# Kernel tuning notes

Hardware: AMD Instinct MI355X
Metric: run time of the kernel (lower is better)

The kernel has to match this reference:

```python
import jax, jax.numpy as jnp
import numpy as np

N_HEADS = 16
SEG = 64
EPS = 1e-6


def _sigma(x):
    # ELU(x) + 1 kernel feature map (strictly positive)
    return jax.nn.elu(x) + 1.0


def setup_inputs() -> dict:
    key = jax.random.key(0)
    kx, kq, kk, kv, ko = jax.random.split(key, 5)
    B, T, D = 4, 4096, 1024
    scale = D ** -0.5
    return {
        "x": jax.random.normal(kx, (B, T, D), dtype=jnp.float32),
        "W_q": jax.random.normal(kq, (D, D), dtype=jnp.float32) * scale,
        "W_k": jax.random.normal(kk, (D, D), dtype=jnp.float32) * scale,
        "W_v": jax.random.normal(kv, (D, D), dtype=jnp.float32) * scale,
        "W_o": jax.random.normal(ko, (D, D), dtype=jnp.float32) * scale,
        "beta_param": jnp.zeros((N_HEADS,), dtype=jnp.float32),
    }


def _infini_attention(x, W_q, W_k, W_v, W_o, beta_param):
    B, T, D = x.shape
    H = N_HEADS
    dk = D // H
    assert T % SEG == 0
    S = T // SEG

    def proj(W):
        # nn.Linear: x @ W.T ; split heads -> (B,H,T,dk) -> (S,B,H,SEG,dk)
        y = (x @ W.T).reshape(B, T, H, dk).transpose(0, 2, 1, 3)
        return y.reshape(B, H, S, SEG, dk).transpose(2, 0, 1, 3, 4)

    Qs, Ks, Vs = proj(W_q), proj(W_k), proj(W_v)

    beta = jax.nn.sigmoid(beta_param).reshape(1, H, 1, 1)
    causal = jnp.triu(jnp.ones((SEG, SEG), dtype=bool), k=1)
    inv_sqrt_dk = 1.0 / jnp.sqrt(jnp.asarray(dk, x.dtype))

    M0 = jnp.zeros((B, H, dk, dk), dtype=x.dtype)
    z0 = jnp.zeros((B, H, dk), dtype=x.dtype)

    def step(carry, qkv):
        M, z = carry
        q, k, v = qkv  # each (B,H,SEG,dk)
        # Eq.4 memory retrieval
        sq = _sigma(q)
        denom_q = jnp.sum(sq * z[:, :, None, :], axis=-1, keepdims=True) + EPS
        A_mem = jnp.matmul(sq, M) / denom_q
        # local causal softmax attention
        scores = jnp.matmul(q, jnp.swapaxes(k, -2, -1)) * inv_sqrt_dk
        scores = jnp.where(causal, -jnp.inf, scores)
        A_dot = jnp.matmul(jax.nn.softmax(scores, axis=-1), v)
        A_s = beta * A_mem + (1.0 - beta) * A_dot
        # Eq.5 delta-rule memory update
        sk = _sigma(k)
        denom_k = jnp.sum(sk * z[:, :, None, :], axis=-1, keepdims=True) + EPS
        V_prev = jnp.matmul(sk, M) / denom_k
        M_new = M + jnp.einsum("bhtk,bhtv->bhkv", sk, v - V_prev)
        z_new = z + jnp.sum(sk, axis=-2)
        return (M_new, z_new), A_s

    (M, z), outs = jax.lax.scan(step, (M0, z0), (Qs, Ks, Vs))
    # outs: (S,B,H,SEG,dk) -> (B,T,D)
    out = outs.transpose(1, 3, 0, 2, 4).reshape(B, S * SEG, H, dk)
    # careful: need segment-major time ordering -> (B, H, T, dk) then (B,T,H,dk)
    out = outs.transpose(1, 2, 0, 3, 4).reshape(B, H, T, dk)
    out = out.transpose(0, 2, 1, 3).reshape(B, T, D)
    out = out @ W_o.T
    return out, M.mean(0), z.mean(0)


def reference(x, W_q, W_k, W_v, W_o, beta_param):
    return _infini_attention(x, W_q, W_k, W_v, W_o, beta_param)
```

## Files before the change

### kernel.cpp

```cpp
#include <hip/hip_runtime.h>

typedef __bf16 bf16_t;
typedef __bf16 bf16x8 __attribute__((ext_vector_type(8)));
typedef __bf16 bf16x4 __attribute__((ext_vector_type(4)));
typedef float  f32x4  __attribute__((ext_vector_type(4)));

#define QKV_STR 3072

__device__ __forceinline__ void gload16(const bf16_t* g, bf16_t* l) {
    __builtin_amdgcn_global_load_lds(
        (const __attribute__((address_space(1))) void*)(g),
        (__attribute__((address_space(3))) void*)(l), 16, 0, 0);
}

__global__ __launch_bounds__(256) void cast_bf16_kernel(const float* __restrict__ in,
                                                        bf16_t* __restrict__ out, int n4) {
    int i = blockIdx.x * 256 + threadIdx.x;
    if (i >= n4) return;
    f32x4 v = *reinterpret_cast<const f32x4*>(in + (size_t)i * 4);
    bf16x4 o;
    o[0] = (bf16_t)v[0]; o[1] = (bf16_t)v[1]; o[2] = (bf16_t)v[2]; o[3] = (bf16_t)v[3];
    *reinterpret_cast<bf16x4*>(out + (size_t)i * 4) = o;
}

__global__ __launch_bounds__(256) void cast4_kernel(const float* __restrict__ w0,
                                                    const float* __restrict__ w1,
                                                    const float* __restrict__ w2,
                                                    const float* __restrict__ w3,
                                                    bf16_t* __restrict__ o0,
                                                    bf16_t* __restrict__ o1,
                                                    bf16_t* __restrict__ o2,
                                                    bf16_t* __restrict__ o3) {
    int which = blockIdx.x >> 10;
    int i = (blockIdx.x & 1023) * 256 + threadIdx.x;
    const float* in = (which == 0) ? w0 : (which == 1) ? w1 : (which == 2) ? w2 : w3;
    bf16_t*     out = (which == 0) ? o0 : (which == 1) ? o1 : (which == 2) ? o2 : o3;
    f32x4 v = *reinterpret_cast<const f32x4*>(in + (size_t)i * 4);
    bf16x4 o;
    o[0] = (bf16_t)v[0]; o[1] = (bf16_t)v[1]; o[2] = (bf16_t)v[2]; o[3] = (bf16_t)v[3];
    *reinterpret_cast<bf16x4*>(out + (size_t)i * 4) = o;
}

__device__ __forceinline__ bf16x8 sigma8(bf16x8 x) {
    bf16x8 o;
#pragma unroll
    for (int j = 0; j < 8; j++) {
        float f = (float)x[j];
        float sg = f > 0.f ? f + 1.f : __expf(f);
        o[j] = (bf16_t)sg;
    }
    return o;
}

template <int OUT_BF16>
__global__ __launch_bounds__(512, 2) void gemm256(const bf16_t* __restrict__ A,
                                                  const bf16_t* __restrict__ Bm,
                                                  void* __restrict__ Cv,
                                                  int M, int N, int K) {
    __shared__ bf16_t As[4][256 * 32];
    __shared__ bf16_t Bs[4][256 * 32];

    int nbn = N >> 8;
    int nwg = (M >> 8) * nbn;
    int bid = blockIdx.x;
    int wg = ((nwg & 7) == 0) ? ((bid & 7) * (nwg >> 3) + (bid >> 3)) : bid;
    int bm = wg / nbn, bn = wg % nbn;

    int tid = threadIdx.x;
    int w = tid >> 6, lane = tid & 63;
    int wm = w >> 2, wn = w & 3;
    int lr = lane & 15, lk = lane >> 4;

    int srow = lane >> 2;
    int schunk = (lane & 3) ^ ((lane >> 3) & 3);
    const bf16_t* gA0 = A  + (size_t)(bm * 256 + w * 32 + srow) * K + schunk * 8;
    const bf16_t* gA1 = gA0 + (size_t)16 * K;
    const bf16_t* gB0 = Bm + (size_t)(bn * 256 + w * 32 + srow) * K + schunk * 8;
    const bf16_t* gB1 = gB0 + (size_t)16 * K;
    int lO0 = (w * 32) * 32 + lane * 8;
    int lO1 = (w * 32 + 16) * 32 + lane * 8;

    int chunkb = (lk ^ ((lr >> 1) & 3)) << 4;
    int aoff[8], boff[4];
#pragma unroll
    for (int mi = 0; mi < 8; mi++) aoff[mi] = (wm * 128 + mi * 16 + lr) * 64 + chunkb;
#pragma unroll
    for (int ni = 0; ni < 4; ni++) boff[ni] = (wn * 64 + ni * 16 + lr) * 64 + chunkb;

    f32x4 acc[8][4];
#pragma unroll
    for (int mi = 0; mi < 8; mi++)
#pragma unroll
        for (int ni = 0; ni < 4; ni++) acc[mi][ni] = (f32x4){0.f, 0.f, 0.f, 0.f};

    const int NT = K >> 5;

    auto STAGE = [&](int t) {
        int slot = t & 3;
        size_t ko = (size_t)t * 32;
        gload16(gA0 + ko, &As[slot][lO0]);
        gload16(gA1 + ko, &As[slot][lO1]);
        gload16(gB0 + ko, &Bs[slot][lO0]);
        gload16(gB1 + ko, &Bs[slot][lO1]);
    };

    STAGE(0); STAGE(1); STAGE(2);

#pragma unroll 1
    for (int t = 0; t < NT; ++t) {
        int ahead = NT - 1 - t;
        if (ahead >= 2)      asm volatile("s_waitcnt vmcnt(8)" ::: "memory");
        else if (ahead == 1) asm volatile("s_waitcnt vmcnt(4)" ::: "memory");
        else                 asm volatile("s_waitcnt vmcnt(0)" ::: "memory");
        __builtin_amdgcn_sched_barrier(0);
        __builtin_amdgcn_s_barrier();
        __builtin_amdgcn_sched_barrier(0);

        const char* pa = (const char*)(&As[t & 3][0]);
        const char* pb = (const char*)(&Bs[t & 3][0]);
        bf16x8 af[8], bfr[4];
#pragma unroll
        for (int mi = 0; mi < 8; mi++)
            af[mi] = *reinterpret_cast<const bf16x8*>(pa + aoff[mi]);
#pragma unroll
        for (int ni = 0; ni < 4; ni++)
            bfr[ni] = *reinterpret_cast<const bf16x8*>(pb + boff[ni]);

        if (t + 3 < NT) STAGE(t + 3);

        asm volatile("s_waitcnt lgkmcnt(0)" ::: "memory");
        __builtin_amdgcn_sched_barrier(0);
        __builtin_amdgcn_s_setprio(1);
#pragma unroll
        for (int mi = 0; mi < 8; mi++)
#pragma unroll
            for (int ni = 0; ni < 4; ni++)
                acc[mi][ni] = __builtin_amdgcn_mfma_f32_16x16x32_bf16(af[mi], bfr[ni], acc[mi][ni], 0, 0, 0);
        __builtin_amdgcn_s_setprio(0);
    }

    int row0 = bm * 256 + wm * 128 + lk * 4;
    int col0 = bn * 256 + wn * 64 + lr;
#pragma unroll
    for (int mi = 0; mi < 8; mi++)
#pragma unroll
        for (int ni = 0; ni < 4; ni++)
#pragma unroll
            for (int jj = 0; jj < 4; jj++) {
                size_t idx = (size_t)(row0 + mi * 16 + jj) * N + (col0 + ni * 16);
                float v = acc[mi][ni][jj];
                if (OUT_BF16) reinterpret_cast<bf16_t*>(Cv)[idx] = (bf16_t)v;
                else          reinterpret_cast<float*>(Cv)[idx]  = v;
            }
}

__global__ __launch_bounds__(256) void attn_kernel(bf16_t* __restrict__ QKV,
                                                   bf16_t* __restrict__ skTg,
                                                   float* __restrict__ csum,
                                                   bf16_t* __restrict__ Adot) {
    __shared__ bf16_t kS[64 * 72];
    __shared__ bf16_t vS[64 * 72];
    __shared__ bf16_t skT[64 * 72];
    __shared__ bf16_t vT[64 * 72];
    __shared__ bf16_t pS[64 * 72];
    __shared__ float  scr[64 * 68];

    int u = blockIdx.x;
    int bh = u >> 6, s = u & 63;
    int b = bh >> 4, h = bh & 15;
    int tid = threadIdx.x;
    int w = tid >> 6, lane = tid & 63;
    int lr = lane & 15, lk = lane >> 4;
    int r = tid >> 2, qd = tid & 3, c0 = qd << 4;

    bf16_t* qp = QKV + (size_t)(b * 4096 + s * 64) * QKV_STR + (size_t)h * 64;
    bf16_t* kp = qp + 1024;
    bf16_t* vp = qp + 2048;
    size_t sb = ((size_t)bh * 64 + s) * 4096;

    {
        bf16x8 k0 = *reinterpret_cast<const bf16x8*>(kp + (size_t)r * QKV_STR + c0);
        bf16x8 k1 = *reinterpret_cast<const bf16x8*>(kp + (size_t)r * QKV_STR + c0 + 8);
        bf16x8 v0 = *reinterpret_cast<const bf16x8*>(vp + (size_t)r * QKV_STR + c0);
        bf16x8 v1 = *reinterpret_cast<const bf16x8*>(vp + (size_t)r * QKV_STR + c0 + 8);
        *reinterpret_cast<bf16x8*>(&kS[r * 72 + c0])     = k0;
        *reinterpret_cast<bf16x8*>(&kS[r * 72 + c0 + 8]) = k1;
        *reinterpret_cast<bf16x8*>(&vS[r * 72 + c0])     = v0;
        *reinterpret_cast<bf16x8*>(&vS[r * 72 + c0 + 8]) = v1;
        bf16x8 s0 = sigma8(k0), s1 = sigma8(k1);
        *reinterpret_cast<bf16x8*>(kp + (size_t)r * QKV_STR + c0)     = s0;
        *reinterpret_cast<bf16x8*>(kp + (size_t)r * QKV_STR + c0 + 8) = s1;
#pragma unroll
        for (int j = 0; j < 8; j++) {
            skT[(c0 + j) * 72 + r]     = s0[j];
            skT[(c0 + 8 + j) * 72 + r] = s1[j];
            vT[(c0 + j) * 72 + r]      = v0[j];
            vT[(c0 + 8 + j) * 72 + r]  = v1[j];
        }
    }
    __syncthreads();

    if (tid < 64) {
        float acc = 0.f;
#pragma unroll 8
        for (int t = 0; t < 64; t++) acc += (float)skT[tid * 72 + t];
        csum[((size_t)bh * 64 + s) * 64 + tid] = acc;
    }
    *reinterpret_cast<bf16x8*>(skTg + sb + (size_t)r * 64 + c0) =
        *reinterpret_cast<const bf16x8*>(&skT[r * 72 + c0]);
    *reinterpret_cast<bf16x8*>(skTg + sb + (size_t)r * 64 + c0 + 8) =
        *reinterpret_cast<const bf16x8*>(&skT[r * 72 + c0 + 8]);
    *reinterpret_cast<bf16x8*>(vp + (size_t)r * QKV_STR + c0) =
        *reinterpret_cast<const bf16x8*>(&vT[r * 72 + c0]);
    *reinterpret_cast<bf16x8*>(vp + (size_t)r * QKV_STR + c0 + 8) =
        *reinterpret_cast<const bf16x8*>(&vT[r * 72 + c0 + 8]);

    {
        bf16x8 aq[2];
#pragma unroll
        for (int ks = 0; ks < 2; ks++)
            aq[ks] = *reinterpret_cast<const bf16x8*>(qp + (size_t)(w * 16 + lr) * QKV_STR + lk * 8 + ks * 32);
        f32x4 sc[4];
#pragma unroll
        for (int ct = 0; ct < 4; ct++) {
            sc[ct] = (f32x4){0.f, 0.f, 0.f, 0.f};
#pragma unroll
            for (int ks = 0; ks < 2; ks++) {
                bf16x8 bfrag = *reinterpret_cast<const bf16x8*>(&kS[(ct * 16 + lr) * 72 + lk * 8 + ks * 32]);
                sc[ct] = __builtin_amdgcn_mfma_f32_16x16x32_bf16(aq[ks], bfrag, sc[ct], 0, 0, 0);
            }
        }
#pragma unroll
        for (int ct = 0; ct < 4; ct++)
#pragma unroll
            for (int j = 0; j < 4; j++)
                scr[(w * 16 + lk * 4 + j) * 68 + ct * 16 + lr] = sc[ct][j] * 0.125f;
    }
    __syncthreads();

    {
        float p[16];
        float mx = -3.4e38f;
        const float* srow_p = &scr[r * 68 + c0];
#pragma unroll
        for (int i = 0; i < 16; i++) {
            int c = c0 + i;
            float v = (c <= r) ? srow_p[i] : -3.4e38f;
            p[i] = v;
            mx = fmaxf(mx, v);
        }
        mx = fmaxf(mx, __shfl_xor(mx, 1));
        mx = fmaxf(mx, __shfl_xor(mx, 2));
        float sum = 0.f;
#pragma unroll
        for (int i = 0; i < 16; i++) {
            int c = c0 + i;
            float e = (c <= r) ? __expf(p[i] - mx) : 0.f;
            p[i] = e;
            sum += e;
        }
        sum += __shfl_xor(sum, 1);
        sum += __shfl_xor(sum, 2);
        float inv = 1.f / sum;
        bf16x8 p0, p1;
#pragma unroll
        for (int j = 0; j < 8; j++) {
            p0[j] = (bf16_t)(p[j] * inv);
            p1[j] = (bf16_t)(p[8 + j] * inv);
        }
        *reinterpret_cast<bf16x8*>(&pS[r * 72 + c0])     = p0;
        *reinterpret_cast<bf16x8*>(&pS[r * 72 + c0 + 8]) = p1;
    }
    __syncthreads();

    {
        f32x4 ad[4];
#pragma unroll
        for (int ct = 0; ct < 4; ct++) {
            ad[ct] = (f32x4){0.f, 0.f, 0.f, 0.f};
#pragma unroll
            for (int ks = 0; ks < 2; ks++) {
                bf16x8 afrag = *reinterpret_cast<const bf16x8*>(&pS[(w * 16 + lr) * 72 + lk * 8 + ks * 32]);
                bf16x8 bfrag = *reinterpret_cast<const bf16x8*>(&vT[(ct * 16 + lr) * 72 + lk * 8 + ks * 32]);
                ad[ct] = __builtin_amdgcn_mfma_f32_16x16x32_bf16(afrag, bfrag, ad[ct], 0, 0, 0);
            }
        }
#pragma unroll
        for (int ct = 0; ct < 4; ct++)
#pragma unroll
            for (int j = 0; j < 4; j++)
                kS[(w * 16 + lk * 4 + j) * 72 + ct * 16 + lr] = (bf16_t)ad[ct][j];
    }
    __syncthreads();
    *reinterpret_cast<bf16x8*>(Adot + sb + (size_t)r * 64 + c0) =
        *reinterpret_cast<const bf16x8*>(&kS[r * 72 + c0]);
    *reinterpret_cast<bf16x8*>(Adot + sb + (size_t)r * 64 + c0 + 8) =
        *reinterpret_cast<const bf16x8*>(&kS[r * 72 + c0 + 8]);
}

__global__ __launch_bounds__(64) void zprefix_kernel(const float* __restrict__ csum,
                                                     float* __restrict__ zx,
                                                     float* __restrict__ zfin) {
    int bh = blockIdx.x;
    int d = threadIdx.x;
    float c[64];
#pragma unroll
    for (int s = 0; s < 64; s++)
        c[s] = csum[((size_t)bh * 64 + s) * 64 + d];
    float z = 0.f;
#pragma unroll
    for (int s = 0; s < 64; s++) {
        zx[((size_t)bh * 64 + s) * 64 + d] = z;
        z += c[s];
    }
    zfin[bh * 64 + d] = z;
}

__global__ __launch_bounds__(128) void denom_kernel(const bf16_t* __restrict__ QKV,
                                                    const float* __restrict__ zx,
                                                    float* __restrict__ invq,
                                                    float* __restrict__ invk) {
    __shared__ float zL[64];
    int u = blockIdx.x;
    int bh = u >> 6, s = u & 63;
    int b = bh >> 4, h = bh & 15;
    int tid = threadIdx.x;
    if (tid < 64) zL[tid] = zx[((size_t)bh * 64 + s) * 64 + tid];
    __syncthreads();
    int row = tid & 63;
    bool isq = tid < 64;
    const bf16_t* src = QKV + (size_t)(b * 4096 + s * 64 + row) * QKV_STR +
                        (size_t)h * 64 + (isq ? 0 : 1024);
    float acc = 0.f;
#pragma unroll
    for (int blk = 0; blk < 8; blk++) {
        bf16x8 v = *reinterpret_cast<const bf16x8*>(src + blk * 8);
#pragma unroll
        for (int j = 0; j < 8; j++) {
            float f = (float)v[j];
            float sg;
            if (isq) {
                sg = f > 0.f ? f + 1.f : __expf(f);
                sg = (float)(bf16_t)sg;
            } else {
                sg = f;
            }
            acc = __builtin_fmaf(sg, zL[blk * 8 + j], acc);
        }
    }
    float inv = 1.f / (acc + 1e-6f);
    float* dst = isq ? invq : invk;
    dst[((size_t)bh * 64 + s) * 64 + row] = inv;
}

__global__ __launch_bounds__(64, 1) void scan_kernel(const bf16_t* __restrict__ QKV,
                                                     const bf16_t* __restrict__ skTg,
                                                     const float* __restrict__ invk,
                                                     bf16_t* __restrict__ Msnap,
                                                     float* __restrict__ Mfin) {
    __shared__ bf16_t MbL[16 * 72];
    __shared__ bf16_t uTL[16 * 72];
    __shared__ float  ikL[64];

    int blk = blockIdx.x;
    int bh = blk & 63, cq = blk >> 6;
    int c0 = cq << 4;
    int b = bh >> 4, h = bh & 15;
    int lane = threadIdx.x;
    int lr = lane & 15, lk = lane >> 4;
    int vr = lane >> 2, vt0 = (lane & 3) << 4;

    const bf16_t* sKb = QKV + 1024;
    const bf16_t* vTb = QKV + 2048;
    size_t chbase = (size_t)(b * 4096) * QKV_STR + (size_t)h * 64;
    size_t stbase = (size_t)bh * 64 * 4096;
    const size_t SEG = (size_t)64 * QKV_STR;

    auto swz = [](bf16_t* base, int row, int intra) -> bf16_t* {
        return (bf16_t*)((char*)base + row * 144 + (intra ^ ((row & 7) << 4)));
    };

    for (int i = lane; i < 16 * 72; i += 64) MbL[i] = (bf16_t)0.f;
    f32x4 Mreg[4];
#pragma unroll
    for (int rt = 0; rt < 4; rt++) Mreg[rt] = (f32x4){0.f, 0.f, 0.f, 0.f};

    bf16x8 cK[4][2], cT[4][2];
#pragma unroll
    for (int rt = 0; rt < 4; rt++)
#pragma unroll
        for (int ks = 0; ks < 2; ks++) {
            cK[rt][ks] = *reinterpret_cast<const bf16x8*>(
                sKb + chbase + (size_t)(rt * 16 + lr) * QKV_STR + lk * 8 + ks * 32);
            cT[rt][ks] = *reinterpret_cast<const bf16x8*>(
                skTg + stbase + (size_t)(rt * 16 + lr) * 64 + lk * 8 + ks * 32);
        }
    {
        bf16x8 v0 = *reinterpret_cast<const bf16x8*>(vTb + chbase + (size_t)(c0 + vr) * QKV_STR + vt0);
        bf16x8 v1 = *reinterpret_cast<const bf16x8*>(vTb + chbase + (size_t)(c0 + vr) * QKV_STR + vt0 + 8);
        *reinterpret_cast<bf16x8*>(swz(uTL, vr, vt0 * 2))      = v0;
        *reinterpret_cast<bf16x8*>(swz(uTL, vr, vt0 * 2 + 16)) = v1;
        ikL[lane] = invk[(size_t)bh * 4096 + lane];
    }

    for (int s = 0; s < 64; s++) {
        bf16x8 nK[4][2], nT[4][2], nv0, nv1;
        float nik = 0.f;
        if (s < 63) {
            size_t vs2 = chbase + (size_t)(s + 1) * SEG;
            size_t sb2 = stbase + (size_t)(s + 1) * 4096;
#pragma unroll
            for (int rt = 0; rt < 4; rt++)
#pragma unroll
                for (int ks = 0; ks < 2; ks++) {
                    nK[rt][ks] = *reinterpret_cast<const bf16x8*>(
                        sKb + vs2 + (size_t)(rt * 16 + lr) * QKV_STR + lk * 8 + ks * 32);
                    nT[rt][ks] = *reinterpret_cast<const bf16x8*>(
                        skTg + sb2 + (size_t)(rt * 16 + lr) * 64 + lk * 8 + ks * 32);
                }
            nv0 = *reinterpret_cast<const bf16x8*>(vTb + vs2 + (size_t)(c0 + vr) * QKV_STR + vt0);
            nv1 = *reinterpret_cast<const bf16x8*>(vTb + vs2 + (size_t)(c0 + vr) * QKV_STR + vt0 + 8);
            nik = invk[(size_t)bh * 4096 + (size_t)(s + 1) * 64 + lane];
        }

        bf16x8 mb0 = *reinterpret_cast<const bf16x8*>(swz(MbL, lr, lk * 16));
        bf16x8 mb1 = *reinterpret_cast<const bf16x8*>(swz(MbL, lr, lk * 16 + 64));
        f32x4 Y[4];
#pragma unroll
        for (int rt = 0; rt < 4; rt++) {
            Y[rt] = (f32x4){0.f, 0.f, 0.f, 0.f};
            Y[rt] = __builtin_amdgcn_mfma_f32_16x16x32_bf16(cK[rt][0], mb0, Y[rt], 0, 0, 0);
            Y[rt] = __builtin_amdgcn_mfma_f32_16x16x32_bf16(cK[rt][1], mb1, Y[rt], 0, 0, 0);
        }

#pragma unroll
        for (int rt = 0; rt < 4; rt++) {
            bf16x4 vv = *reinterpret_cast<const bf16x4*>(swz(uTL, lr, rt * 32 + lk * 8));
            bf16x4 uu;
#pragma unroll
            for (int j = 0; j < 4; j++) {
                float ik = ikL[rt * 16 + lk * 4 + j];
                uu[j] = (bf16_t)((float)vv[j] - Y[rt][j] * ik);
            }
            *reinterpret_cast<bf16x4*>(swz(uTL, lr, rt * 32 + lk * 8)) = uu;
        }

        bf16x8 ub0 = *reinterpret_cast<const bf16x8*>(swz(uTL, lr, lk * 16));
        bf16x8 ub1 = *reinterpret_cast<const bf16x8*>(swz(uTL, lr, lk * 16 + 64));
#pragma unroll
        for (int rt = 0; rt < 4; rt++) {
            Mreg[rt] = __builtin_amdgcn_mfma_f32_16x16x32_bf16(cT[rt][0], ub0, Mreg[rt], 0, 0, 0);
            Mreg[rt] = __builtin_amdgcn_mfma_f32_16x16x32_bf16(cT[rt][1], ub1, Mreg[rt], 0, 0, 0);
        }

#pragma unroll
        for (int rt = 0; rt < 4; rt++) {
            bf16x4 mp;
#pragma unroll
            for (int j = 0; j < 4; j++) mp[j] = (bf16_t)Mreg[rt][j];
            *reinterpret_cast<bf16x4*>(swz(MbL, lr, rt * 32 + lk * 8)) = mp;
            if (s < 63)
                *reinterpret_cast<bf16x4*>(
                    Msnap + (((size_t)bh * 64 + s + 1) * 64 + c0 + lr) * 64 + rt * 16 + lk * 4) = mp;
        }

        if (s < 63) {
#pragma unroll
            for (int rt = 0; rt < 4; rt++)
#pragma unroll
                for (int ks = 0; ks < 2; ks++) { cK[rt][ks] = nK[rt][ks]; cT[rt][ks] = nT[rt][ks]; }
            *reinterpret_cast<bf16x8*>(swz(uTL, vr, vt0 * 2))      = nv0;
            *reinterpret_cast<bf16x8*>(swz(uTL, vr, vt0 * 2 + 16)) = nv1;
            ikL[lane] = nik;
        }
    }

#pragma unroll
    for (int rt = 0; rt < 4; rt++)
#pragma unroll
        for (int j = 0; j < 4; j++)
            Mfin[(size_t)bh * 4096 + (size_t)(rt * 16 + lk * 4 + j) * 64 + c0 + lr] = Mreg[rt][j];
}

__global__ __launch_bounds__(256) void combine_kernel(const bf16_t* __restrict__ QKV,
                                                      const bf16_t* __restrict__ Msnap,
                                                      const bf16_t* __restrict__ Adot,
                                                      const float* __restrict__ invq,
                                                      const float* __restrict__ beta_param,
                                                      bf16_t* __restrict__ Op) {
    __shared__ bf16_t oS[64 * 72];
    __shared__ bf16_t adS[64 * 72];
    __shared__ float  iq[64];

    int u = blockIdx.x;
    int bh = u >> 6, s = u & 63;
    int b = bh >> 4, h = bh & 15;
    int tid = threadIdx.x;
    int w = tid >> 6, lane = tid & 63;
    int lr = lane & 15, lk = lane >> 4;
    int r = tid >> 2, c0 = (tid & 3) << 4;

    const bf16_t* qp = QKV + (size_t)(b * 4096 + s * 64) * QKV_STR + (size_t)h * 64;
    size_t vsegO = ((size_t)b * 4096 + s * 64) * 1024 + (size_t)h * 64;
    size_t sb = ((size_t)bh * 64 + s) * 4096;
    size_t ib = ((size_t)bh * 64 + s) * 64;

    float beta = 1.f / (1.f + __expf(-beta_param[h]));
    float omb = 1.f - beta;

    *reinterpret_cast<bf16x8*>(&adS[r * 72 + c0]) =
        *reinterpret_cast<const bf16x8*>(Adot + sb + (size_t)r * 64 + c0);
    *reinterpret_cast<bf16x8*>(&adS[r * 72 + c0 + 8]) =
        *reinterpret_cast<const bf16x8*>(Adot + sb + (size_t)r * 64 + c0 + 8);
    if (tid < 64) iq[tid] = invq[ib + tid];

    f32x4 Y[4];
#pragma unroll
    for (int ct = 0; ct < 4; ct++) Y[ct] = (f32x4){0.f, 0.f, 0.f, 0.f};
    if (s > 0) {
        bf16x8 aq[2];
#pragma unroll
        for (int ks = 0; ks < 2; ks++)
            aq[ks] = sigma8(*reinterpret_cast<const bf16x8*>(
                qp + (size_t)(w * 16 + lr) * QKV_STR + lk * 8 + ks * 32));
#pragma unroll
        for (int ct = 0; ct < 4; ct++)
#pragma unroll
            for (int ks = 0; ks < 2; ks++) {
                bf16x8 bfrag = *reinterpret_cast<const bf16x8*>(
                    Msnap + sb + (size_t)(ct * 16 + lr) * 64 + lk * 8 + ks * 32);
                Y[ct] = __builtin_amdgcn_mfma_f32_16x16x32_bf16(aq[ks], bfrag, Y[ct], 0, 0, 0);
            }
    }
    __syncthreads();

#pragma unroll
    for (int ct = 0; ct < 4; ct++) {
        int colc = ct * 16 + lr;
#pragma unroll
        for (int j = 0; j < 4; j++) {
            int t = w * 16 + lk * 4 + j;
            float o = beta * (Y[ct][j] * iq[t]) + omb * (float)adS[t * 72 + colc];
            oS[t * 72 + colc] = (bf16_t)o;
        }
    }
    __syncthreads();

    *reinterpret_cast<bf16x8*>(Op + vsegO + (size_t)r * 1024 + c0) =
        *reinterpret_cast<const bf16x8*>(&oS[r * 72 + c0]);
    *reinterpret_cast<bf16x8*>(Op + vsegO + (size_t)r * 1024 + c0 + 8) =
        *reinterpret_cast<const bf16x8*>(&oS[r * 72 + c0 + 8]);
}

__global__ __launch_bounds__(256) void mean_kernel(const float* __restrict__ Mfin,
                                                   const float* __restrict__ zfin,
                                                   float* __restrict__ out) {
    int idx = blockIdx.x * 256 + threadIdx.x;
    if (idx < 65536) {
        out[16777216 + idx] = 0.25f * (Mfin[idx] + Mfin[idx + 65536] +
                                       Mfin[idx + 131072] + Mfin[idx + 196608]);
    } else if (idx < 66560) {
        int j = idx - 65536;
        out[16842752 + j] = 0.25f * (zfin[j] + zfin[j + 1024] + zfin[j + 2048] + zfin[j + 3072]);
    }
}

extern "C" void kernel_launch(void* const* d_in, const int* in_sizes, int n_in,
                              void* d_out, int out_size, void* d_ws, size_t ws_size,
                              hipStream_t stream) {
    const float* x      = (const float*)d_in[0];
    const float* Wq     = (const float*)d_in[1];
    const float* Wk     = (const float*)d_in[2];
    const float* Wv     = (const float*)d_in[3];
    const float* Wo     = (const float*)d_in[4];
    const float* beta_p = (const float*)d_in[5];
    float* out = (float*)d_out;
    char* ws = (char*)d_ws;

    const size_t NX = 16777216ull;

    bf16_t* xb   = (bf16_t*)ws;
    bf16_t* Adot = xb;
    bf16_t* Wqb  = (bf16_t*)(ws + 33554432);
    bf16_t* Wkb  = (bf16_t*)(ws + 35651584);
    bf16_t* Wvb  = (bf16_t*)(ws + 37748736);
    bf16_t* Wob  = (bf16_t*)(ws + 39845888);
    bf16_t* QKV  = (bf16_t*)(ws + 41943040);
    bf16_t* skT  = (bf16_t*)(ws + 142606336);
    bf16_t* Op   = (bf16_t*)(ws + 176160768);
    float*  csum = (float*)(ws + 209715200);
    float*  zx   = (float*)(ws + 210763776);
    float*  invq = (float*)(ws + 211812352);
    float*  invk = (float*)(ws + 212860928);
    float*  Mfin = (float*)(ws + 213909504);
    float*  zfin = (float*)(ws + 214958080);
    bf16_t* Msnap = (bf16_t*)d_out;

    cast_bf16_kernel<<<dim3(16384), dim3(256), 0, stream>>>(x, xb, (int)(NX / 4));
    cast4_kernel<<<dim3(4096), dim3(256), 0, stream>>>(Wq, Wk, Wv, Wo, Wqb, Wkb, Wvb, Wob);

    gemm256<1><<<dim3(768), dim3(512), 0, stream>>>(xb, Wqb, (void*)QKV, 16384, 3072, 1024);

    attn_kernel<<<dim3(4096), dim3(256), 0, stream>>>(QKV, skT, csum, Adot);
    zprefix_kernel<<<dim3(64), dim3(64), 0, stream>>>(csum, zx, zfin);
    denom_kernel<<<dim3(4096), dim3(128), 0, stream>>>(QKV, zx, invq, invk);
    scan_kernel<<<dim3(256), dim3(64), 0, stream>>>(QKV, skT, invk, Msnap, Mfin);
    combine_kernel<<<dim3(4096), dim3(256), 0, stream>>>(QKV, Msnap, Adot, invq, beta_p, Op);

    gemm256<0><<<dim3(256), dim3(512), 0, stream>>>(Op, Wob, d_out, 16384, 1024, 1024);
    mean_kernel<<<dim3(260), dim3(256), 0, stream>>>(Mfin, zfin, out);
}
```

Before: 337.9 us.

## Fuse query denominator into combine kernel and relax GEMM LDS wait

The sigma(q)·z denominator is now computed inside combine_kernel, reusing the sigma(q) fragments it already loads and reducing across lanes with shuffles. The separate denominator kernel shrinks to a 64-thread key-only version, which removes the invq buffer round trip and half of that kernel's QKV reads. In the GEMM main loop, the B fragments are now loaded before the A fragments and the explicit lgkmcnt(0) wait and its sched barrier are dropped. This lets the compiler place finer-grained waits so MFMAs can start before every LDS read has landed. The combine kernel gains an extra __syncthreads and some per-block arithmetic.

Result: faster. 318.2 us (-5.8%).

```diff
diff --git a/kernel.cpp b/kernel.cpp
--- a/kernel.cpp
+++ b/kernel.cpp
@@ -120,16 +120,14 @@
         const char* pb = (const char*)(&Bs[t & 3][0]);
         bf16x8 af[8], bfr[4];
 #pragma unroll
+        for (int ni = 0; ni < 4; ni++)
+            bfr[ni] = *reinterpret_cast<const bf16x8*>(pb + boff[ni]);
+#pragma unroll
         for (int mi = 0; mi < 8; mi++)
             af[mi] = *reinterpret_cast<const bf16x8*>(pa + aoff[mi]);
-#pragma unroll
-        for (int ni = 0; ni < 4; ni++)
-            bfr[ni] = *reinterpret_cast<const bf16x8*>(pb + boff[ni]);
 
         if (t + 3 < NT) STAGE(t + 3);
 
-        asm volatile("s_waitcnt lgkmcnt(0)" ::: "memory");
-        __builtin_amdgcn_sched_barrier(0);
         __builtin_amdgcn_s_setprio(1);
 #pragma unroll
         for (int mi = 0; mi < 8; mi++)
@@ -316,41 +314,27 @@
     zfin[bh * 64 + d] = z;
 }
 
-__global__ __launch_bounds__(128) void denom_kernel(const bf16_t* __restrict__ QKV,
+__global__ __launch_bounds__(64) void denomk_kernel(const bf16_t* __restrict__ QKV,
                                                     const float* __restrict__ zx,
-                                                    float* __restrict__ invq,
                                                     float* __restrict__ invk) {
     __shared__ float zL[64];
     int u = blockIdx.x;
     int bh = u >> 6, s = u & 63;
     int b = bh >> 4, h = bh & 15;
     int tid = threadIdx.x;
-    if (tid < 64) zL[tid] = zx[((size_t)bh * 64 + s) * 64 + tid];
-    __syncthreads();
-    int row = tid & 63;
-    bool isq = tid < 64;
-    const bf16_t* src = QKV + (size_t)(b * 4096 + s * 64 + row) * QKV_STR +
-                        (size_t)h * 64 + (isq ? 0 : 1024);
+    zL[tid] = zx[((size_t)bh * 64 + s) * 64 + tid];
+    __syncthreads();
+    const bf16_t* src = QKV + (size_t)(b * 4096 + s * 64 + tid) * QKV_STR +
+                        (size_t)h * 64 + 1024;
     float acc = 0.f;
 #pragma unroll
     for (int blk = 0; blk < 8; blk++) {
         bf16x8 v = *reinterpret_cast<const bf16x8*>(src + blk * 8);
 #pragma unroll
-        for (int j = 0; j < 8; j++) {
-            float f = (float)v[j];
-            float sg;
-            if (isq) {
-                sg = f > 0.f ? f + 1.f : __expf(f);
-                sg = (float)(bf16_t)sg;
-            } else {
-                sg = f;
-            }
-            acc = __builtin_fmaf(sg, zL[blk * 8 + j], acc);
-        }
-    }
-    float inv = 1.f / (acc + 1e-6f);
-    float* dst = isq ? invq : invk;
-    dst[((size_t)bh * 64 + s) * 64 + row] = inv;
+        for (int j = 0; j < 8; j++)
+            acc = __builtin_fmaf((float)v[j], zL[blk * 8 + j], acc);
+    }
+    invk[((size_t)bh * 64 + s) * 64 + tid] = 1.f / (acc + 1e-6f);
 }
 
 __global__ __launch_bounds__(64, 1) void scan_kernel(const bf16_t* __restrict__ QKV,
@@ -485,12 +469,13 @@
 __global__ __launch_bounds__(256) void combine_kernel(const bf16_t* __restrict__ QKV,
                                                       const bf16_t* __restrict__ Msnap,
                                                       const bf16_t* __restrict__ Adot,
-                                                      const float* __restrict__ invq,
+                                                      const float* __restrict__ zx,
                                                       const float* __restrict__ beta_param,
                                                       bf16_t* __restrict__ Op) {
     __shared__ bf16_t oS[64 * 72];
     __shared__ bf16_t adS[64 * 72];
     __shared__ float  iq[64];
+    __shared__ float  zL[64];
 
     int u = blockIdx.x;
     int bh = u >> 6, s = u & 63;
@@ -512,7 +497,11 @@
         *reinterpret_cast<const bf16x8*>(Adot + sb + (size_t)r * 64 + c0);
     *reinterpret_cast<bf16x8*>(&adS[r * 72 + c0 + 8]) =
         *reinterpret_cast<const bf16x8*>(Adot + sb + (size_t)r * 64 + c0 + 8);
-    if (tid < 64) iq[tid] = invq[ib + tid];
+    if (tid < 64) {
+        zL[tid] = zx[ib + tid];
+        iq[tid] = 0.f;
+    }
+    __syncthreads();
 
     f32x4 Y[4];
 #pragma unroll
@@ -523,6 +512,15 @@
         for (int ks = 0; ks < 2; ks++)
             aq[ks] = sigma8(*reinterpret_cast<const bf16x8*>(
                 qp + (size_t)(w * 16 + lr) * QKV_STR + lk * 8 + ks * 32));
+        float dq = 0.f;
+#pragma unroll
+        for (int ks = 0; ks < 2; ks++)
+#pragma unroll
+            for (int j = 0; j < 8; j++)
+                dq = __builtin_fmaf((float)aq[ks][j], zL[ks * 32 + lk * 8 + j], dq);
+        dq += __shfl_xor(dq, 16);
+        dq += __shfl_xor(dq, 32);
+        if (lk == 0) iq[w * 16 + lr] = 1.f / (dq + 1e-6f);
 #pragma unroll
         for (int ct = 0; ct < 4; ct++)
 #pragma unroll
@@ -590,7 +588,6 @@
     bf16_t* Op   = (bf16_t*)(ws + 176160768);
     float*  csum = (float*)(ws + 209715200);
     float*  zx   = (float*)(ws + 210763776);
-    float*  invq = (float*)(ws + 211812352);
     float*  invk = (float*)(ws + 212860928);
     float*  Mfin = (float*)(ws + 213909504);
     float*  zfin = (float*)(ws + 214958080);
@@ -603,9 +600,9 @@
 
     attn_kernel<<<dim3(4096), dim3(256), 0, stream>>>(QKV, skT, csum, Adot);
     zprefix_kernel<<<dim3(64), dim3(64), 0, stream>>>(csum, zx, zfin);
-    denom_kernel<<<dim3(4096), dim3(128), 0, stream>>>(QKV, zx, invq, invk);
+    denomk_kernel<<<dim3(4096), dim3(64), 0, stream>>>(QKV, zx, invk);
     scan_kernel<<<dim3(256), dim3(64), 0, stream>>>(QKV, skT, invk, Msnap, Mfin);
-    combine_kernel<<<dim3(4096), dim3(256), 0, stream>>>(QKV, Msnap, Adot, invq, beta_p, Op);
+    combine_kernel<<<dim3(4096), dim3(256), 0, stream>>>(QKV, Msnap, Adot, zx, beta_p, Op);
 
     gemm256<0><<<dim3(256), dim3(512), 0, stream>>>(Op, Wob, d_out, 16384, 1024, 1024);
     mean_kernel<<<dim3(260), dim3(256), 0, stream>>>(Mfin, zfin, out);
```
